# Optimization experiments

Hardware: AMD Instinct MI355X
Metric: run time of the kernel (lower is better)

Reference implementation:

```python
import jax, jax.numpy as jnp
import numpy as np

N = 4096; E = 4096
IN_DIM = 256; H1 = 128; H2 = 128; H3 = 64; OUT = 16
NH1 = 2; NH2 = 2; ALPHA = 0.2
TDIMS = [933, 303, 683, 798]  # per-timepoint raw dims (nomal_linear1..4)
TP = 4; GRU_IN = 2 * OUT; GRU_H = 128


def _leaky(x, s):
    return jnp.where(x >= 0, x, s * x)


def _att_layer(x, mask, W, a, b):
    # GAT-style: h = xW; e = leaky(Wh1 + Wh2^T); adjacency-masked softmax; aggregate
    h = x @ W                                   # [N, d]
    d = W.shape[-1]
    e = _leaky((h @ a[:d])[:, None] + (h @ a[d:])[None, :], ALPHA)  # [N, N]
    att = jax.nn.softmax(jnp.where(mask, e, -9e15), axis=1)
    out = _leaky(att @ h, ALPHA)
    out = out / jnp.maximum(jnp.linalg.norm(out, axis=1, keepdims=True), 1e-12)
    return out + b

_multi_head = jax.vmap(_att_layer, in_axes=(None, None, 0, 0, 0))


def _encode(x, mask, W1, a1, b1, W2, a2, b2):
    x = jax.nn.elu(jnp.mean(_multi_head(x, mask, W1, a1, b1), axis=0))
    # second conv layer runs under torch.no_grad() in the original
    return jax.lax.stop_gradient(jnp.mean(_multi_head(x, mask, W2, a2, b2), axis=0))


def _gru_layer(xs, wih, whh, bih, bhh):
    # xs: [T, B, in]; torch GRU gate order (r, z, n)
    B = xs.shape[1]
    def step(h, xt):
        gi = xt @ wih + bih
        gh = h @ whh + bhh
        ir, iz, inn = jnp.split(gi, 3, axis=-1)
        hr, hz, hn = jnp.split(gh, 3, axis=-1)
        r = jax.nn.sigmoid(ir + hr)
        z = jax.nn.sigmoid(iz + hz)
        n = jnp.tanh(inn + r * hn)
        h_new = (1.0 - z) * n + z * h
        return h_new, h_new
    _, ys = jax.lax.scan(step, jnp.zeros((B, GRU_H), xs.dtype), xs)
    return ys


def setup_inputs() -> dict:
    key = jax.random.key(0)
    ks = iter(jax.random.split(key, 80))
    def rn(shape, s=0.05):
        return jax.random.normal(next(ks), shape, dtype=jnp.float32) * s
    inp = {}
    for i, d in enumerate(TDIMS):
        inp['x%d' % i] = rn((N, d), 1.0)
    inp['adj'] = jax.random.randint(next(ks), (N, N), 0, 2, dtype=jnp.int32)
    inp['train_sample'] = jax.random.randint(next(ks), (E, 2), 0, N)
    for i, d in enumerate(TDIMS):
        inp['nw%d' % i] = rn((d, IN_DIM))
        inp['nb%d' % i] = jnp.zeros((IN_DIM,), jnp.float32)
    inp['W1'] = rn((NH1, IN_DIM, H1)); inp['a1'] = rn((NH1, 2 * H1)); inp['b1'] = jnp.zeros((NH1, H1), jnp.float32)
    inp['W2'] = rn((NH2, H1, H2));     inp['a2'] = rn((NH2, 2 * H2)); inp['b2'] = jnp.zeros((NH2, H2), jnp.float32)
    inp['tfw1'] = rn((H2, H3)); inp['tfb1'] = jnp.zeros((H3,), jnp.float32)
    inp['tfw2'] = rn((H3, OUT)); inp['tfb2'] = jnp.zeros((OUT,), jnp.float32)
    inp['tgw1'] = rn((H2, H3)); inp['tgb1'] = jnp.zeros((H3,), jnp.float32)
    inp['tgw2'] = rn((H3, OUT)); inp['tgb2'] = jnp.zeros((OUT,), jnp.float32)
    inp['wih0'] = rn((GRU_IN, 3 * GRU_H)); inp['whh0'] = rn((GRU_H, 3 * GRU_H))
    inp['bih0'] = jnp.zeros((3 * GRU_H,), jnp.float32); inp['bhh0'] = jnp.zeros((3 * GRU_H,), jnp.float32)
    inp['wih1'] = rn((GRU_H, 3 * GRU_H)); inp['whh1'] = rn((GRU_H, 3 * GRU_H))
    inp['bih1'] = jnp.zeros((3 * GRU_H,), jnp.float32); inp['bhh1'] = jnp.zeros((3 * GRU_H,), jnp.float32)
    inp['attw'] = rn((GRU_H, GRU_H)); inp['attb'] = jnp.zeros((GRU_H,), jnp.float32)
    inp['fow'] = rn((GRU_H, 1)); inp['fob'] = jnp.zeros((1,), jnp.float32)
    return inp


def reference(x0, x1, x2, x3, adj, train_sample,
              nw0, nb0, nw1, nb1, nw2, nb2, nw3, nb3,
              W1, a1, b1, W2, a2, b2,
              tfw1, tfb1, tfw2, tfb2, tgw1, tgb1, tgw2, tgb2,
              wih0, whh0, bih0, bhh0, wih1, whh1, bih1, bhh1,
              attw, attb, fow, fob):
    mask = adj > 0
    xs = (x0, x1, x2, x3)
    nws = ((nw0, nb0), (nw1, nb1), (nw2, nb2), (nw3, nb3))
    tf_idx = train_sample[:, 0]
    tg_idx = train_sample[:, 1]
    steps = []
    for i in range(TP):  # fixed small loop over time points
        w, b = nws[i]
        e = xs[i] @ w + b                       # per-timepoint projection to input_dim
        embed = _encode(e, mask, W1, a1, b1, W2, a2, b2)
        # dropout (p=0.01) treated as identity for a deterministic reference
        tf = _leaky(_leaky(embed @ tfw1 + tfb1, 0.01) @ tfw2 + tfb2, 0.01)
        tg = _leaky(_leaky(embed @ tgw1 + tgb1, 0.01) @ tgw2 + tgb2, 0.01)
        steps.append(jnp.concatenate([tf[tf_idx], tg[tg_idx]], axis=1))  # [E, 32]
    h_x = jnp.stack(steps, axis=0)              # [T, E, 32]
    y0 = _gru_layer(h_x, wih0, whh0, bih0, bhh0)            # [T, E, 128]
    r_out = jnp.transpose(_gru_layer(y0, wih1, whh1, bih1, bhh1), (1, 0, 2))  # [E, T, 128]
    aw = jax.nn.softmax(r_out @ attw + attb, axis=1)        # softmax over time dim
    att_out = jnp.sum(aw * r_out, axis=1)                   # [E, 128]
    return att_out @ fow + fob                              # [E, 1]
```

## Files before the change

### kernel.cpp

```cpp
#include <hip/hip_runtime.h>
#include <cstdint>
#include <cstddef>

#define NN 4096
#define DH 128
#define TP 4
#define ATT_S 4
#define ATT_BM 64

typedef _Float16 f16x8 __attribute__((ext_vector_type(8)));
typedef float f32x4 __attribute__((ext_vector_type(4)));

__global__ __launch_bounds__(256) void pack_mask_k(const int* __restrict__ adj,
                                                   unsigned long long* __restrict__ mb) {
  int w = blockIdx.x * 4 + (threadIdx.x >> 6);
  int lane = threadIdx.x & 63;
  int v = adj[(size_t)w * 64 + lane];
  unsigned long long bits = __ballot(v > 0);
  if (lane == 0) mb[w] = bits;
}

__global__ __launch_bounds__(256) void fill0_k(float* __restrict__ p, int n) {
  int i = blockIdx.x * 256 + threadIdx.x;
  if (i < n) p[i] = 0.f;
}

template <int ACT>
__global__ __launch_bounds__(256) void gemm_mfma_k(const float* __restrict__ A, const float* __restrict__ B,
                                                   const float* __restrict__ bias, float* __restrict__ C,
                                                   int M, int N, int K) {
  __shared__ _Float16 AH[64 * 64], AL[64 * 64];
  __shared__ _Float16 BH[64 * 64], BL[64 * 64];
  const int tid = threadIdx.x;
  const int bm = blockIdx.y * 64, bn = blockIdx.x * 64;
  const int arow = tid >> 2, akc = (tid & 3) * 16;
  const int bcol = tid & 63, bkc = (tid >> 6) * 16;
  const int w = tid >> 6, lane = tid & 63;
  const int wm = w >> 1, wn = w & 1;
  const int l15 = lane & 15, l4 = lane >> 4;
  f32x4 acc[2][2] = {};

  for (int k0 = 0; k0 < K; k0 += 64) {
    __syncthreads();
    {
      const float* ar = A + (size_t)(bm + arow) * K;
      f16x8 hv[2], lv[2];
#pragma unroll
      for (int e = 0; e < 16; e++) {
        int gk = k0 + akc + e;
        float v = (gk < K) ? ar[gk] : 0.f;
        _Float16 hi = (_Float16)v;
        hv[e >> 3][e & 7] = hi;
        lv[e >> 3][e & 7] = (_Float16)(v - (float)hi);
      }
#pragma unroll
      for (int hf = 0; hf < 2; hf++) {
        int byt = ((arow * 64 + akc + hf * 8) * 2) ^ ((arow & 7) << 4);
        *(f16x8*)((char*)AH + byt) = hv[hf];
        *(f16x8*)((char*)AL + byt) = lv[hf];
      }
    }
    {
      f16x8 hv[2], lv[2];
      const bool cok = (bn + bcol) < N;
#pragma unroll
      for (int e = 0; e < 16; e++) {
        int gk = k0 + bkc + e;
        float v = (gk < K && cok) ? B[(size_t)gk * N + bn + bcol] : 0.f;
        _Float16 hi = (_Float16)v;
        hv[e >> 3][e & 7] = hi;
        lv[e >> 3][e & 7] = (_Float16)(v - (float)hi);
      }
#pragma unroll
      for (int hf = 0; hf < 2; hf++) {
        int byt = ((bcol * 64 + bkc + hf * 8) * 2) ^ ((bcol & 7) << 4);
        *(f16x8*)((char*)BH + byt) = hv[hf];
        *(f16x8*)((char*)BL + byt) = lv[hf];
      }
    }
    __syncthreads();
#pragma unroll
    for (int kf = 0; kf < 2; kf++) {
      f16x8 ah[2], al[2], bh[2], bl[2];
#pragma unroll
      for (int m2 = 0; m2 < 2; m2++) {
        int r = wm * 32 + m2 * 16 + l15;
        int byt = ((r * 64 + kf * 32 + l4 * 8) * 2) ^ ((r & 7) << 4);
        ah[m2] = *(const f16x8*)((const char*)AH + byt);
        al[m2] = *(const f16x8*)((const char*)AL + byt);
      }
#pragma unroll
      for (int nf = 0; nf < 2; nf++) {
        int c = wn * 32 + nf * 16 + l15;
        int byt = ((c * 64 + kf * 32 + l4 * 8) * 2) ^ ((c & 7) << 4);
        bh[nf] = *(const f16x8*)((const char*)BH + byt);
        bl[nf] = *(const f16x8*)((const char*)BL + byt);
      }
#pragma unroll
      for (int m2 = 0; m2 < 2; m2++)
#pragma unroll
        for (int nf = 0; nf < 2; nf++) {
          acc[m2][nf] = __builtin_amdgcn_mfma_f32_16x16x32_f16(ah[m2], bh[nf], acc[m2][nf], 0, 0, 0);
          acc[m2][nf] = __builtin_amdgcn_mfma_f32_16x16x32_f16(ah[m2], bl[nf], acc[m2][nf], 0, 0, 0);
          acc[m2][nf] = __builtin_amdgcn_mfma_f32_16x16x32_f16(al[m2], bh[nf], acc[m2][nf], 0, 0, 0);
        }
    }
  }
#pragma unroll
  for (int m2 = 0; m2 < 2; m2++)
#pragma unroll
    for (int nf = 0; nf < 2; nf++) {
      int c = bn + wn * 32 + nf * 16 + l15;
      if (c < N) {
        float bv = bias ? bias[c] : 0.f;
#pragma unroll
        for (int q = 0; q < 4; q++) {
          int r = bm + wm * 32 + m2 * 16 + l4 * 4 + q;
          float v = acc[m2][nf][q] + bv;
          if (ACT == 1) v = (v >= 0.f) ? v : 0.01f * v;
          C[(size_t)r * N + c] = v;
        }
      }
    }
}

__global__ __launch_bounds__(256) void eler_k(const float* __restrict__ h0p, const float* __restrict__ h1p,
                                              const float* __restrict__ a,
                                              float* __restrict__ el, float* __restrict__ er) {
  int head = blockIdx.y;
  const float* h = head ? h1p : h0p;
  const float* ah = a + (size_t)head * 256;
  int row = blockIdx.x * 4 + (threadIdx.x >> 6);
  int lane = threadIdx.x & 63;
  const float* hr = h + (size_t)row * DH;
  float h0 = hr[lane], h1 = hr[lane + 64];
  float pe = h0 * ah[lane] + h1 * ah[lane + 64];
  float pr = h0 * ah[128 + lane] + h1 * ah[192 + lane];
#pragma unroll
  for (int off = 32; off >= 1; off >>= 1) {
    pe += __shfl_xor(pe, off, 64);
    pr += __shfl_xor(pr, off, 64);
  }
  if (lane == 0) { el[(size_t)head * NN + row] = pe; er[(size_t)head * NN + row] = pr; }
}

__global__ __launch_bounds__(256) void rowmax_k(const float* __restrict__ el, const float* __restrict__ er,
                                                const unsigned long long* __restrict__ mb,
                                                float* __restrict__ mrow) {
  int head = blockIdx.y;
  int row = blockIdx.x * 4 + (threadIdx.x >> 6);
  int lane = threadIdx.x & 63;
  const float* erh = er + (size_t)head * NN;
  const unsigned long long* mr = mb + (size_t)row * 64;
  float mx = -INFINITY;
  for (int i = 0; i < 64; i++) {
    unsigned long long w = mr[i];
    float v = erh[i * 64 + lane];
    mx = fmaxf(mx, ((w >> lane) & 1ull) ? v : -INFINITY);
  }
#pragma unroll
  for (int off = 32; off >= 1; off >>= 1) mx = fmaxf(mx, __shfl_xor(mx, off, 64));
  if (lane == 0) {
    float s = el[(size_t)head * NN + row] + mx;
    mrow[(size_t)head * NN + row] = fmaxf(s, 0.2f * s);
  }
}

__global__ __launch_bounds__(256) void gat_mfma_k(const float* __restrict__ h0p, const float* __restrict__ h1p,
                                                  const float* __restrict__ el, const float* __restrict__ er,
                                                  const float* __restrict__ mrow,
                                                  const unsigned long long* __restrict__ mb,
                                                  float* __restrict__ Opart, float* __restrict__ Zpart) {
  const int split = blockIdx.x;
  const int mblk = blockIdx.y;
  const int head = blockIdx.z;
  const float* h = head ? h1p : h0p;
  const float* elh = el + (size_t)head * NN;
  const float* erh = er + (size_t)head * NN;
  const float* mh = mrow + (size_t)head * NN;
  float* Op = Opart + ((size_t)head * ATT_S + split) * NN * DH;
  float* Zp = Zpart + ((size_t)head * ATT_S + split) * NN;

  __shared__ _Float16 PH[ATT_BM * 64];
  __shared__ _Float16 PL[ATT_BM * 64];
  __shared__ _Float16 HH[128 * 64];
  __shared__ _Float16 HL[128 * 64];
  __shared__ float zred[ATT_BM][4];

  const int tid = threadIdx.x;
  const int prow = tid >> 2;
  const int pk0 = (tid & 3) * 16;
  const int grow = mblk * ATT_BM + prow;
  const float el_r = elh[grow];
  const float m_r = mh[grow];
  const int sc = tid & 127;
  const int skh = tid >> 7;
  const int w = tid >> 6, lane = tid & 63;
  const int wm = w >> 1, wn = w & 1;
  const int l15 = lane & 15, l4 = lane >> 4;

  f32x4 acc[2][4] = {};
  float zacc = 0.f;
  const int jbase = split * (NN / ATT_S);

  for (int jt = 0; jt < NN / ATT_S; jt += 64) {
    const int j0 = jbase + jt;
    __syncthreads();

#pragma unroll
    for (int kq = 0; kq < 4; kq++) {
      int k = skh * 32 + kq * 8;
      f16x8 hv, lv;
#pragma unroll
      for (int e = 0; e < 8; e++) {
        float v = h[(size_t)(j0 + k + e) * DH + sc];
        _Float16 hi = (_Float16)v;
        hv[e] = hi;
        lv[e] = (_Float16)(v - (float)hi);
      }
      int byt = ((sc * 64 + k) * 2) ^ ((sc & 7) << 4);
      *(f16x8*)((char*)HH + byt) = hv;
      *(f16x8*)((char*)HL + byt) = lv;
    }

    {
      unsigned long long wbits = mb[(size_t)grow * 64 + (j0 >> 6)];
      float er_v[16];
#pragma unroll
      for (int q = 0; q < 4; q++) {
        float4 t = *(const float4*)&erh[j0 + pk0 + q * 4];
        er_v[q * 4 + 0] = t.x; er_v[q * 4 + 1] = t.y;
        er_v[q * 4 + 2] = t.z; er_v[q * 4 + 3] = t.w;
      }
      f16x8 hv[2], lv[2];
#pragma unroll
      for (int e = 0; e < 16; e++) {
        float sr = el_r + er_v[e];
        float s = fmaxf(sr, 0.2f * sr);
        float p = ((wbits >> (pk0 + e)) & 1ull) ? __expf(s - m_r) : 0.f;
        zacc += p;
        _Float16 hi = (_Float16)p;
        hv[e >> 3][e & 7] = hi;
        lv[e >> 3][e & 7] = (_Float16)(p - (float)hi);
      }
#pragma unroll
      for (int half = 0; half < 2; half++) {
        int byt = (((prow * 64) + pk0 + half * 8) * 2) ^ ((prow & 7) << 4);
        *(f16x8*)((char*)PH + byt) = hv[half];
        *(f16x8*)((char*)PL + byt) = lv[half];
      }
    }
    __syncthreads();

#pragma unroll
    for (int kf = 0; kf < 2; kf++) {
      f16x8 ah[2], al[2];
#pragma unroll
      for (int m2 = 0; m2 < 2; m2++) {
        int ar = wm * 32 + m2 * 16 + l15;
        int ak = kf * 32 + l4 * 8;
        int ab = ((ar * 64 + ak) * 2) ^ ((ar & 7) << 4);
        ah[m2] = *(const f16x8*)((const char*)PH + ab);
        al[m2] = *(const f16x8*)((const char*)PL + ab);
      }
#pragma unroll
      for (int nf = 0; nf < 4; nf++) {
        int bc = wn * 64 + nf * 16 + l15;
        int bk = kf * 32 + l4 * 8;
        int bb = ((bc * 64 + bk) * 2) ^ ((bc & 7) << 4);
        f16x8 bh = *(const f16x8*)((const char*)HH + bb);
        f16x8 bl = *(const f16x8*)((const char*)HL + bb);
#pragma unroll
        for (int m2 = 0; m2 < 2; m2++) {
          acc[m2][nf] = __builtin_amdgcn_mfma_f32_16x16x32_f16(ah[m2], bh, acc[m2][nf], 0, 0, 0);
          acc[m2][nf] = __builtin_amdgcn_mfma_f32_16x16x32_f16(ah[m2], bl, acc[m2][nf], 0, 0, 0);
          acc[m2][nf] = __builtin_amdgcn_mfma_f32_16x16x32_f16(al[m2], bh, acc[m2][nf], 0, 0, 0);
        }
      }
    }
  }

  zred[prow][tid & 3] = zacc;
  __syncthreads();
  if (tid < ATT_BM) {
    float z = zred[tid][0] + zred[tid][1] + zred[tid][2] + zred[tid][3];
    Zp[mblk * ATT_BM + tid] = z;
  }

#pragma unroll
  for (int m2 = 0; m2 < 2; m2++)
#pragma unroll
    for (int nf = 0; nf < 4; nf++)
#pragma unroll
      for (int q = 0; q < 4; q++) {
        int r = mblk * ATT_BM + wm * 32 + m2 * 16 + l4 * 4 + q;
        int c = wn * 64 + nf * 16 + l15;
        Op[(size_t)r * DH + c] = acc[m2][nf][q];
      }
}

template <int DO_ELU>
__global__ __launch_bounds__(256) void combine_k(const float* __restrict__ Opart,
                                                 const float* __restrict__ Zpart,
                                                 const float* __restrict__ bvec,
                                                 float* __restrict__ out) {
  int row = blockIdx.x * 4 + (threadIdx.x >> 6);
  int lane = threadIdx.x & 63;
  int c = lane * 2;
  float o0 = 0.f, o1 = 0.f;
#pragma unroll
  for (int hd = 0; hd < 2; hd++) {
    float a0 = 0.f, a1 = 0.f, Z = 0.f;
#pragma unroll
    for (int s = 0; s < ATT_S; s++) {
      const float* Op = Opart + ((size_t)hd * ATT_S + s) * NN * DH;
      float2 t = *(const float2*)&Op[(size_t)row * DH + c];
      a0 += t.x; a1 += t.y;
      Z += Zpart[((size_t)hd * ATT_S + s) * NN + row];
    }
    float invZ = 1.f / Z;
    float v0 = a0 * invZ, v1 = a1 * invZ;
    v0 = fmaxf(v0, 0.2f * v0);
    v1 = fmaxf(v1, 0.2f * v1);
    float ss = v0 * v0 + v1 * v1;
#pragma unroll
    for (int off = 32; off >= 1; off >>= 1) ss += __shfl_xor(ss, off, 64);
    float sc_ = 1.f / fmaxf(sqrtf(ss), 1e-12f);
    o0 += 0.5f * (v0 * sc_ + bvec[hd * DH + c]);
    o1 += 0.5f * (v1 * sc_ + bvec[hd * DH + c + 1]);
  }
  if (DO_ELU) {
    o0 = (o0 > 0.f) ? o0 : expm1f(o0);
    o1 = (o1 > 0.f) ? o1 : expm1f(o1);
  }
  float2 st = {o0, o1};
  *(float2*)&out[(size_t)row * DH + c] = st;
}

__global__ __launch_bounds__(256) void gather_k(const float* __restrict__ tf, const float* __restrict__ tg,
                                                const int* __restrict__ ts, float* __restrict__ hx_t) {
  int idx = blockIdx.x * 256 + threadIdx.x;
  int e = idx >> 5, c = idx & 31;
  int src = (c < 16) ? ts[e * 2] : ts[e * 2 + 1];
  float v = (c < 16) ? tf[(size_t)src * 16 + c] : tg[(size_t)src * 16 + (c - 16)];
  hx_t[idx] = v;
}

__global__ __launch_bounds__(256) void gru_gate_k(const float* __restrict__ gi, const float* __restrict__ gh,
                                                  const float* __restrict__ hprev, float* __restrict__ hout) {
  int idx = blockIdx.x * 256 + threadIdx.x;
  int b = idx >> 7, c = idx & 127;
  const float* gib = gi + (size_t)b * 384;
  const float* ghb = gh + (size_t)b * 384;
  float ir = gib[c], iz = gib[128 + c], in_ = gib[256 + c];
  float hr = ghb[c], hz = ghb[128 + c], hn = ghb[256 + c];
  float rr = 1.f / (1.f + __expf(-(ir + hr)));
  float zz = 1.f / (1.f + __expf(-(iz + hz)));
  float nn_ = tanhf(in_ + rr * hn);
  hout[idx] = (1.f - zz) * nn_ + zz * hprev[idx];
}

__global__ __launch_bounds__(256) void attpool_k(const float* __restrict__ z, const float* __restrict__ y,
                                                 float* __restrict__ o) {
  int idx = blockIdx.x * 256 + threadIdx.x;
  const size_t S = (size_t)NN * DH;
  float z0 = z[idx], z1 = z[idx + S], z2 = z[idx + 2 * S], z3 = z[idx + 3 * S];
  float mx = fmaxf(fmaxf(z0, z1), fmaxf(z2, z3));
  float e0 = __expf(z0 - mx), e1 = __expf(z1 - mx), e2 = __expf(z2 - mx), e3 = __expf(z3 - mx);
  float inv = 1.f / (e0 + e1 + e2 + e3);
  o[idx] = (e0 * y[idx] + e1 * y[idx + S] + e2 * y[idx + 2 * S] + e3 * y[idx + 3 * S]) * inv;
}

__global__ __launch_bounds__(256) void final_k(const float* __restrict__ at, const float* __restrict__ fow,
                                               const float* __restrict__ fob, float* __restrict__ out) {
  int row = blockIdx.x * 4 + (threadIdx.x >> 6);
  int lane = threadIdx.x & 63;
  const float* ar = at + (size_t)row * DH;
  float p = ar[lane] * fow[lane] + ar[lane + 64] * fow[lane + 64];
#pragma unroll
  for (int off = 32; off >= 1; off >>= 1) p += __shfl_xor(p, off, 64);
  if (lane == 0) out[row] = p + fob[0];
}

static inline void run_gemm(int act, const float* A, const float* B, const float* bias, float* C,
                            int M, int N, int K, hipStream_t s) {
  dim3 g((N + 63) / 64, M / 64), b(256);
  if (act == 0) gemm_mfma_k<0><<<g, b, 0, s>>>(A, B, bias, C, M, N, K);
  else          gemm_mfma_k<1><<<g, b, 0, s>>>(A, B, bias, C, M, N, K);
}

extern "C" void kernel_launch(void* const* d_in, const int* in_sizes, int n_in,
                              void* d_out, int out_size, void* d_ws, size_t ws_size,
                              hipStream_t stream) {
  const float* x[4]  = {(const float*)d_in[0], (const float*)d_in[1], (const float*)d_in[2], (const float*)d_in[3]};
  const int* adj     = (const int*)d_in[4];
  const int* tsample = (const int*)d_in[5];
  const float* nw[4] = {(const float*)d_in[6], (const float*)d_in[8], (const float*)d_in[10], (const float*)d_in[12]};
  const float* nb[4] = {(const float*)d_in[7], (const float*)d_in[9], (const float*)d_in[11], (const float*)d_in[13]};
  const float* W1 = (const float*)d_in[14];
  const float* a1 = (const float*)d_in[15];
  const float* b1 = (const float*)d_in[16];
  const float* W2 = (const float*)d_in[17];
  const float* a2 = (const float*)d_in[18];
  const float* b2 = (const float*)d_in[19];
  const float* tfw1 = (const float*)d_in[20]; const float* tfb1 = (const float*)d_in[21];
  const float* tfw2 = (const float*)d_in[22]; const float* tfb2 = (const float*)d_in[23];
  const float* tgw1 = (const float*)d_in[24]; const float* tgb1 = (const float*)d_in[25];
  const float* tgw2 = (const float*)d_in[26]; const float* tgb2 = (const float*)d_in[27];
  const float* wih0 = (const float*)d_in[28]; const float* whh0 = (const float*)d_in[29];
  const float* bih0 = (const float*)d_in[30]; const float* bhh0 = (const float*)d_in[31];
  const float* wih1 = (const float*)d_in[32]; const float* whh1 = (const float*)d_in[33];
  const float* bih1 = (const float*)d_in[34]; const float* bhh1 = (const float*)d_in[35];
  const float* attw = (const float*)d_in[36]; const float* attb = (const float*)d_in[37];
  const float* fow  = (const float*)d_in[38]; const float* fob  = (const float*)d_in[39];
  float* out = (float*)d_out;

  char* base = (char*)d_ws;
  size_t off = 0;
  auto alloc = [&](size_t bytes) -> void* {
    void* p = base + off;
    off += (bytes + 255) & ~(size_t)255;
    return p;
  };
  const size_t SN = (size_t)NN * DH;
  unsigned long long* mbits = (unsigned long long*)alloc((size_t)NN * 64 * 8);
  float* ebuf = (float*)alloc((size_t)NN * 256 * 4);
  float* h0   = (float*)alloc(SN * 4);
  float* h1   = (float*)alloc(SN * 4);
  float* el   = (float*)alloc((size_t)2 * NN * 4);
  float* er   = (float*)alloc((size_t)2 * NN * 4);
  float* mrowb= (float*)alloc((size_t)2 * NN * 4);
  float* bufA = (float*)alloc(SN * 4);
  float* bufB = (float*)alloc(SN * 4);
  float* tmp1 = (float*)alloc((size_t)NN * 64 * 4);
  float* tfb_ = (float*)alloc((size_t)NN * 16 * 4);
  float* tgb_ = (float*)alloc((size_t)NN * 16 * 4);
  float* hx   = (float*)alloc((size_t)TP * NN * 32 * 4);
  float* y0   = (float*)alloc((size_t)TP * SN * 4);
  float* y1   = (float*)alloc((size_t)TP * SN * 4);
  float* gi   = (float*)alloc((size_t)NN * 384 * 4);
  float* gh   = (float*)alloc((size_t)NN * 384 * 4);
  float* Opart = y0;
  float* Zpart = gi;
  float* zatt   = gi;
  float* zbuf   = ebuf;
  float* attout = h0;

  const int TD[4] = {933, 303, 683, 798};

  pack_mask_k<<<(NN * 64) / 4, 256, 0, stream>>>(adj, mbits);

  for (int t = 0; t < TP; t++) {
    run_gemm(0, x[t], nw[t], nb[t], ebuf, NN, 256, TD[t], stream);

    run_gemm(0, ebuf, W1, nullptr, h0, NN, DH, 256, stream);
    run_gemm(0, ebuf, W1 + (size_t)256 * DH, nullptr, h1, NN, DH, 256, stream);
    eler_k<<<dim3(NN / 4, 2), 256, 0, stream>>>(h0, h1, a1, el, er);
    rowmax_k<<<dim3(NN / 4, 2), 256, 0, stream>>>(el, er, mbits, mrowb);
    gat_mfma_k<<<dim3(ATT_S, NN / ATT_BM, 2), 256, 0, stream>>>(h0, h1, el, er, mrowb, mbits, Opart, Zpart);
    combine_k<1><<<NN / 4, 256, 0, stream>>>(Opart, Zpart, b1, bufB);

    run_gemm(0, bufB, W2, nullptr, h0, NN, DH, DH, stream);
    run_gemm(0, bufB, W2 + (size_t)DH * DH, nullptr, h1, NN, DH, DH, stream);
    eler_k<<<dim3(NN / 4, 2), 256, 0, stream>>>(h0, h1, a2, el, er);
    rowmax_k<<<dim3(NN / 4, 2), 256, 0, stream>>>(el, er, mbits, mrowb);
    gat_mfma_k<<<dim3(ATT_S, NN / ATT_BM, 2), 256, 0, stream>>>(h0, h1, el, er, mrowb, mbits, Opart, Zpart);
    combine_k<0><<<NN / 4, 256, 0, stream>>>(Opart, Zpart, b2, bufA);

    run_gemm(1, bufA, tfw1, tfb1, tmp1, NN, 64, DH, stream);
    run_gemm(1, tmp1, tfw2, tfb2, tfb_, NN, 16, 64, stream);
    run_gemm(1, bufA, tgw1, tgb1, tmp1, NN, 64, DH, stream);
    run_gemm(1, tmp1, tgw2, tgb2, tgb_, NN, 16, 64, stream);
    gather_k<<<(NN * 32) / 256, 256, 0, stream>>>(tfb_, tgb_, tsample, hx + (size_t)t * NN * 32);
  }

  fill0_k<<<(int)(SN / 256), 256, 0, stream>>>(zbuf, (int)SN);

  for (int t = 0; t < TP; t++) {
    const float* hprev = (t == 0) ? zbuf : (y0 + (size_t)(t - 1) * SN);
    run_gemm(0, hx + (size_t)t * NN * 32, wih0, bih0, gi, NN, 384, 32, stream);
    run_gemm(0, hprev, whh0, bhh0, gh, NN, 384, DH, stream);
    gru_gate_k<<<(int)(SN / 256), 256, 0, stream>>>(gi, gh, hprev, y0 + (size_t)t * SN);
  }
  for (int t = 0; t < TP; t++) {
    const float* hprev = (t == 0) ? zbuf : (y1 + (size_t)(t - 1) * SN);
    run_gemm(0, y0 + (size_t)t * SN, wih1, bih1, gi, NN, 384, DH, stream);
    run_gemm(0, hprev, whh1, bhh1, gh, NN, 384, DH, stream);
    gru_gate_k<<<(int)(SN / 256), 256, 0, stream>>>(gi, gh, hprev, y1 + (size_t)t * SN);
  }

  run_gemm(0, y1, attw, attb, zatt, TP * NN, DH, DH, stream);
  attpool_k<<<(int)(SN / 256), 256, 0, stream>>>(zatt, y1, attout);
  final_k<<<NN / 4, 256, 0, stream>>>(attout, fow, fob, out);
}
```

Measured before the change: 1.556 ms.

## Precompute split-fp16 H tiles once and fuse per-head projections

Adds a hsplit kernel that converts each head's projected features into swizzled fp16 hi/lo tiles once per layer. The attention kernel then copies those tiles with vector loads instead of re-reading fp32 H and re-splitting it in every split and row block. The two per-head projection GEMMs are merged into one launch writing a concatenated buffer. The GRU's zero-hidden first step skips the hh GEMM and the zero-fill. This costs an extra kernel and an fp16 tile buffer in exchange for removing redundant conversion work in the hot attention loop.

```diff
diff --git a/kernel.cpp b/kernel.cpp
--- a/kernel.cpp
+++ b/kernel.cpp
@@ -20,12 +20,7 @@
   if (lane == 0) mb[w] = bits;
 }
 
-__global__ __launch_bounds__(256) void fill0_k(float* __restrict__ p, int n) {
-  int i = blockIdx.x * 256 + threadIdx.x;
-  if (i < n) p[i] = 0.f;
-}
-
-template <int ACT>
+template <int ACT, int BHEAD>
 __global__ __launch_bounds__(256) void gemm_mfma_k(const float* __restrict__ A, const float* __restrict__ B,
                                                    const float* __restrict__ bias, float* __restrict__ C,
                                                    int M, int N, int K) {
@@ -40,6 +35,11 @@
   const int l15 = lane & 15, l4 = lane >> 4;
   f32x4 acc[2][2] = {};
 
+  const float* Bp = B;
+  int bcb = bn;
+  if (BHEAD) { int hd = bn >> 7; Bp = B + (size_t)hd * K * 128; bcb = bn & 127; }
+  const int ldb = BHEAD ? 128 : N;
+
   for (int k0 = 0; k0 < K; k0 += 64) {
     __syncthreads();
     {
@@ -62,11 +62,11 @@
     }
     {
       f16x8 hv[2], lv[2];
-      const bool cok = (bn + bcol) < N;
+      const bool cok = (bcb + bcol) < ldb;
 #pragma unroll
       for (int e = 0; e < 16; e++) {
         int gk = k0 + bkc + e;
-        float v = (gk < K && cok) ? B[(size_t)gk * N + bn + bcol] : 0.f;
+        float v = (gk < K && cok) ? Bp[(size_t)gk * ldb + bcb + bcol] : 0.f;
         _Float16 hi = (_Float16)v;
         hv[e >> 3][e & 7] = hi;
         lv[e >> 3][e & 7] = (_Float16)(v - (float)hi);
@@ -124,15 +124,13 @@
     }
 }
 
-__global__ __launch_bounds__(256) void eler_k(const float* __restrict__ h0p, const float* __restrict__ h1p,
-                                              const float* __restrict__ a,
+__global__ __launch_bounds__(256) void eler_k(const float* __restrict__ hcat, const float* __restrict__ a,
                                               float* __restrict__ el, float* __restrict__ er) {
   int head = blockIdx.y;
-  const float* h = head ? h1p : h0p;
   const float* ah = a + (size_t)head * 256;
   int row = blockIdx.x * 4 + (threadIdx.x >> 6);
   int lane = threadIdx.x & 63;
-  const float* hr = h + (size_t)row * DH;
+  const float* hr = hcat + (size_t)row * 256 + head * 128;
   float h0 = hr[lane], h1 = hr[lane + 64];
   float pe = h0 * ah[lane] + h1 * ah[lane + 64];
   float pr = h0 * ah[128 + lane] + h1 * ah[192 + lane];
@@ -166,7 +164,32 @@
   }
 }
 
-__global__ __launch_bounds__(256) void gat_mfma_k(const float* __restrict__ h0p, const float* __restrict__ h1p,
+__global__ __launch_bounds__(256) void hsplit_k(const float* __restrict__ hcat,
+                                                _Float16* __restrict__ HTH, _Float16* __restrict__ HTL) {
+  const int jblk = blockIdx.x;
+  const int head = blockIdx.y;
+  const int tid = threadIdx.x;
+  const int c = tid & 127;
+  const size_t tileBase = ((size_t)head * (NN / 64) + jblk) * 8192;
+#pragma unroll
+  for (int kq = 0; kq < 4; kq++) {
+    int k0 = (tid >> 7) * 32 + kq * 8;
+    f16x8 hv, lv;
+#pragma unroll
+    for (int e = 0; e < 8; e++) {
+      float v = hcat[(size_t)(jblk * 64 + k0 + e) * 256 + head * 128 + c];
+      _Float16 hi = (_Float16)v;
+      hv[e] = hi;
+      lv[e] = (_Float16)(v - (float)hi);
+    }
+    int byt = ((c * 64 + k0) * 2) ^ ((c & 7) << 4);
+    *(f16x8*)((char*)(HTH + tileBase) + byt) = hv;
+    *(f16x8*)((char*)(HTL + tileBase) + byt) = lv;
+  }
+}
+
+__global__ __launch_bounds__(256) void gat_mfma_k(const _Float16* __restrict__ HTH_g,
+                                                  const _Float16* __restrict__ HTL_g,
                                                   const float* __restrict__ el, const float* __restrict__ er,
                                                   const float* __restrict__ mrow,
                                                   const unsigned long long* __restrict__ mb,
@@ -174,7 +197,6 @@
   const int split = blockIdx.x;
   const int mblk = blockIdx.y;
   const int head = blockIdx.z;
-  const float* h = head ? h1p : h0p;
   const float* elh = el + (size_t)head * NN;
   const float* erh = er + (size_t)head * NN;
   const float* mh = mrow + (size_t)head * NN;
@@ -193,8 +215,6 @@
   const int grow = mblk * ATT_BM + prow;
   const float el_r = elh[grow];
   const float m_r = mh[grow];
-  const int sc = tid & 127;
-  const int skh = tid >> 7;
   const int w = tid >> 6, lane = tid & 63;
   const int wm = w >> 1, wn = w & 1;
   const int l15 = lane & 15, l4 = lane >> 4;
@@ -205,26 +225,20 @@
 
   for (int jt = 0; jt < NN / ATT_S; jt += 64) {
     const int j0 = jbase + jt;
+    const int jblk = j0 >> 6;
+    const char* srcH = (const char*)(HTH_g + ((size_t)head * (NN / 64) + jblk) * 8192);
+    const char* srcL = (const char*)(HTL_g + ((size_t)head * (NN / 64) + jblk) * 8192);
     __syncthreads();
 
-#pragma unroll
-    for (int kq = 0; kq < 4; kq++) {
-      int k = skh * 32 + kq * 8;
-      f16x8 hv, lv;
-#pragma unroll
-      for (int e = 0; e < 8; e++) {
-        float v = h[(size_t)(j0 + k + e) * DH + sc];
-        _Float16 hi = (_Float16)v;
-        hv[e] = hi;
-        lv[e] = (_Float16)(v - (float)hi);
-      }
-      int byt = ((sc * 64 + k) * 2) ^ ((sc & 7) << 4);
-      *(f16x8*)((char*)HH + byt) = hv;
-      *(f16x8*)((char*)HL + byt) = lv;
+    f16x8 rh[4], rl[4];
+#pragma unroll
+    for (int i = 0; i < 4; i++) {
+      rh[i] = *(const f16x8*)(srcH + (tid + i * 256) * 16);
+      rl[i] = *(const f16x8*)(srcL + (tid + i * 256) * 16);
     }
 
     {
-      unsigned long long wbits = mb[(size_t)grow * 64 + (j0 >> 6)];
+      unsigned long long wbits = mb[(size_t)grow * 64 + jblk];
       float er_v[16];
 #pragma unroll
       for (int q = 0; q < 4; q++) {
@@ -249,6 +263,12 @@
         *(f16x8*)((char*)PH + byt) = hv[half];
         *(f16x8*)((char*)PL + byt) = lv[half];
       }
+    }
+
+#pragma unroll
+    for (int i = 0; i < 4; i++) {
+      *(f16x8*)((char*)HH + (tid + i * 256) * 16) = rh[i];
+      *(f16x8*)((char*)HL + (tid + i * 256) * 16) = rl[i];
     }
     __syncthreads();
 
@@ -360,6 +380,19 @@
   hout[idx] = (1.f - zz) * nn_ + zz * hprev[idx];
 }
 
+__global__ __launch_bounds__(256) void gru_gate0_k(const float* __restrict__ gi, const float* __restrict__ bhh,
+                                                   float* __restrict__ hout) {
+  int idx = blockIdx.x * 256 + threadIdx.x;
+  int b = idx >> 7, c = idx & 127;
+  const float* gib = gi + (size_t)b * 384;
+  float ir = gib[c], iz = gib[128 + c], in_ = gib[256 + c];
+  float hr = bhh[c], hz = bhh[128 + c], hn = bhh[256 + c];
+  float rr = 1.f / (1.f + __expf(-(ir + hr)));
+  float zz = 1.f / (1.f + __expf(-(iz + hz)));
+  float nn_ = tanhf(in_ + rr * hn);
+  hout[idx] = (1.f - zz) * nn_;
+}
+
 __global__ __launch_bounds__(256) void attpool_k(const float* __restrict__ z, const float* __restrict__ y,
                                                  float* __restrict__ o) {
   int idx = blockIdx.x * 256 + threadIdx.x;
@@ -385,8 +418,11 @@
 static inline void run_gemm(int act, const float* A, const float* B, const float* bias, float* C,
                             int M, int N, int K, hipStream_t s) {
   dim3 g((N + 63) / 64, M / 64), b(256);
-  if (act == 0) gemm_mfma_k<0><<<g, b, 0, s>>>(A, B, bias, C, M, N, K);
-  else          gemm_mfma_k<1><<<g, b, 0, s>>>(A, B, bias, C, M, N, K);
+  if (act == 0) gemm_mfma_k<0, 0><<<g, b, 0, s>>>(A, B, bias, C, M, N, K);
+  else          gemm_mfma_k<1, 0><<<g, b, 0, s>>>(A, B, bias, C, M, N, K);
+}
+static inline void run_proj(const float* A, const float* B, float* C, int K, hipStream_t s) {
+  gemm_mfma_k<0, 1><<<dim3(4, NN / 64), 256, 0, s>>>(A, B, nullptr, C, NN, 256, K);
 }
 
 extern "C" void kernel_launch(void* const* d_in, const int* in_sizes, int n_in,
@@ -425,8 +461,7 @@
   const size_t SN = (size_t)NN * DH;
   unsigned long long* mbits = (unsigned long long*)alloc((size_t)NN * 64 * 8);
   float* ebuf = (float*)alloc((size_t)NN * 256 * 4);
-  float* h0   = (float*)alloc(SN * 4);
-  float* h1   = (float*)alloc(SN * 4);
+  float* hcat = (float*)alloc((size_t)NN * 256 * 4);
   float* el   = (float*)alloc((size_t)2 * NN * 4);
   float* er   = (float*)alloc((size_t)2 * NN * 4);
   float* mrowb= (float*)alloc((size_t)2 * NN * 4);
@@ -443,8 +478,9 @@
   float* Opart = y0;
   float* Zpart = gi;
   float* zatt   = gi;
-  float* zbuf   = ebuf;
-  float* attout = h0;
+  float* attout = hcat;
+  _Float16* HTH = (_Float16*)ebuf;
+  _Float16* HTL = HTH + (size_t)2 * NN * 128;
 
   const int TD[4] = {933, 303, 683, 798};
 
@@ -453,18 +489,18 @@
   for (int t = 0; t < TP; t++) {
     run_gemm(0, x[t], nw[t], nb[t], ebuf, NN, 256, TD[t], stream);
 
-    run_gemm(0, ebuf, W1, nullptr, h0, NN, DH, 256, stream);
-    run_gemm(0, ebuf, W1 + (size_t)256 * DH, nullptr, h1, NN, DH, 256, stream);
-    eler_k<<<dim3(NN / 4, 2), 256, 0, stream>>>(h0, h1, a1, el, er);
+    run_proj(ebuf, W1, hcat, 256, stream);
+    hsplit_k<<<dim3(NN / 64, 2), 256, 0, stream>>>(hcat, HTH, HTL);
+    eler_k<<<dim3(NN / 4, 2), 256, 0, stream>>>(hcat, a1, el, er);
     rowmax_k<<<dim3(NN / 4, 2), 256, 0, stream>>>(el, er, mbits, mrowb);
-    gat_mfma_k<<<dim3(ATT_S, NN / ATT_BM, 2), 256, 0, stream>>>(h0, h1, el, er, mrowb, mbits, Opart, Zpart);
+    gat_mfma_k<<<dim3(ATT_S, NN / ATT_BM, 2), 256, 0, stream>>>(HTH, HTL, el, er, mrowb, mbits, Opart, Zpart);
     combine_k<1><<<NN / 4, 256, 0, stream>>>(Opart, Zpart, b1, bufB);
 
-    run_gemm(0, bufB, W2, nullptr, h0, NN, DH, DH, stream);
-    run_gemm(0, bufB, W2 + (size_t)DH * DH, nullptr, h1, NN, DH, DH, stream);
-    eler_k<<<dim3(NN / 4, 2), 256, 0, stream>>>(h0, h1, a2, el, er);
+    run_proj(bufB, W2, hcat, 128, stream);
+    hsplit_k<<<dim3(NN / 64, 2), 256, 0, stream>>>(hcat, HTH, HTL);
+    eler_k<<<dim3(NN / 4, 2), 256, 0, stream>>>(hcat, a2, el, er);
     rowmax_k<<<dim3(NN / 4, 2), 256, 0, stream>>>(el, er, mbits, mrowb);
-    gat_mfma_k<<<dim3(ATT_S, NN / ATT_BM, 2), 256, 0, stream>>>(h0, h1, el, er, mrowb, mbits, Opart, Zpart);
+    gat_mfma_k<<<dim3(ATT_S, NN / ATT_BM, 2), 256, 0, stream>>>(HTH, HTL, el, er, mrowb, mbits, Opart, Zpart);
     combine_k<0><<<NN / 4, 256, 0, stream>>>(Opart, Zpart, b2, bufA);
 
     run_gemm(1, bufA, tfw1, tfb1, tmp1, NN, 64, DH, stream);
@@ -474,16 +510,18 @@
     gather_k<<<(NN * 32) / 256, 256, 0, stream>>>(tfb_, tgb_, tsample, hx + (size_t)t * NN * 32);
   }
 
-  fill0_k<<<(int)(SN / 256), 256, 0, stream>>>(zbuf, (int)SN);
-
-  for (int t = 0; t < TP; t++) {
-    const float* hprev = (t == 0) ? zbuf : (y0 + (size_t)(t - 1) * SN);
+  run_gemm(0, hx, wih0, bih0, gi, NN, 384, 32, stream);
+  gru_gate0_k<<<(int)(SN / 256), 256, 0, stream>>>(gi, bhh0, y0);
+  for (int t = 1; t < TP; t++) {
+    const float* hprev = y0 + (size_t)(t - 1) * SN;
     run_gemm(0, hx + (size_t)t * NN * 32, wih0, bih0, gi, NN, 384, 32, stream);
     run_gemm(0, hprev, whh0, bhh0, gh, NN, 384, DH, stream);
     gru_gate_k<<<(int)(SN / 256), 256, 0, stream>>>(gi, gh, hprev, y0 + (size_t)t * SN);
   }
-  for (int t = 0; t < TP; t++) {
-    const float* hprev = (t == 0) ? zbuf : (y1 + (size_t)(t - 1) * SN);
+  run_gemm(0, y0, wih1, bih1, gi, NN, 384, DH, stream);
+  gru_gate0_k<<<(int)(SN / 256), 256, 0, stream>>>(gi, bhh1, y1);
+  for (int t = 1; t < TP; t++) {
+    const float* hprev = y1 + (size_t)(t - 1) * SN;
     run_gemm(0, y0 + (size_t)t * SN, wih1, bih1, gi, NN, 384, DH, stream);
     run_gemm(0, hprev, whh1, bhh1, gh, NN, 384, DH, stream);
     gru_gate_k<<<(int)(SN / 256), 256, 0, stream>>>(gi, gh, hprev, y1 + (size_t)t * SN);
```

After: 1.356 ms. 12.9% less time.
